# Optimization experiments

Hardware: AMD Instinct MI355X
Metric: run time of the kernel (lower is better)

Reference implementation:

```python
import jax, jax.numpy as jnp
import numpy as np

NUM_HEADS = 16
NUM_EXPERTS = 8
TOP_K = 2
LN_EPS = 1e-5


def _layernorm(x, g, b):
    mu = x.mean(-1, keepdims=True)
    var = ((x - mu) ** 2).mean(-1, keepdims=True)
    return (x - mu) * jax.lax.rsqrt(var + LN_EPS) * g + b


def _rope(x, cos, sin):
    # x: [B,S,H,D]; cos/sin: [S, D//2]; interleaved even/odd pairs
    B, S, H, D = x.shape
    xr = x.reshape(B, S, H, D // 2, 2)
    xe, xo = xr[..., 0], xr[..., 1]
    c = cos[None, :, None, :]
    s = sin[None, :, None, :]
    ye = xe * c - xo * s
    yo = xe * s + xo * c
    return jnp.stack((ye, yo), axis=-1).reshape(B, S, H, D)


def setup_inputs() -> dict:
    key = jax.random.key(0)
    ks = jax.random.split(key, 8)
    B, S, D = 4, 512, 1024
    E, Hd = NUM_EXPERTS, 1792
    sc = 0.02
    return {
        'x': jax.random.normal(ks[0], (B, S, D), jnp.float32),
        'ln1_g': jnp.ones((D,), jnp.float32),
        'ln1_b': jnp.zeros((D,), jnp.float32),
        'ln2_g': jnp.ones((D,), jnp.float32),
        'ln2_b': jnp.zeros((D,), jnp.float32),
        'w_qkv': jax.random.normal(ks[1], (D, 3 * D), jnp.float32) * sc,
        'w_o': jax.random.normal(ks[2], (D, D), jnp.float32) * sc,
        'gate_w': jax.random.normal(ks[3], (D, E), jnp.float32) * sc,
        'w_gate': jax.random.normal(ks[4], (E, D, Hd), jnp.float32) * sc,
        'w_up': jax.random.normal(ks[5], (E, D, Hd), jnp.float32) * sc,
        'w_down': jax.random.normal(ks[6], (E, Hd, D), jnp.float32) * sc,
    }


def reference(x, ln1_g, ln1_b, ln2_g, ln2_b, w_qkv, w_o, gate_w, w_gate, w_up, w_down):
    B, S, D = x.shape
    H = NUM_HEADS
    hd = D // H

    # --- attention with RoPE ---
    xn = _layernorm(x, ln1_g, ln1_b)
    qkv = xn @ w_qkv                      # [B,S,3D]
    q, k, v = jnp.split(qkv, 3, axis=-1)
    q = q.reshape(B, S, H, hd)
    k = k.reshape(B, S, H, hd)
    v = v.reshape(B, S, H, hd)
    inv_freq = 1.0 / (10000.0 ** (jnp.arange(0, hd, 2, dtype=jnp.float32) / hd))
    t = jnp.arange(S, dtype=jnp.float32)
    freqs = jnp.outer(t, inv_freq)        # [S, hd//2]
    cos, sin = jnp.cos(freqs), jnp.sin(freqs)
    q = _rope(q, cos, sin)
    k = _rope(k, cos, sin)
    scale = 1.0 / jnp.sqrt(jnp.asarray(hd, x.dtype))
    scores = jnp.einsum('bshd,bthd->bhst', q, k) * scale
    causal = jnp.tril(jnp.ones((S, S), bool))
    scores = jnp.where(causal[None, None], scores, jnp.finfo(scores.dtype).min)
    attn = jax.nn.softmax(scores, axis=-1)
    attn_out = jnp.einsum('bhst,bthd->bshd', attn, v).reshape(B, S, D)
    x = x + attn_out @ w_o

    # --- MoE ---
    xn2 = _layernorm(x, ln2_g, ln2_b)
    xf = xn2.reshape(-1, D)               # [T, D]
    logits = (xf.astype(jnp.bfloat16) @ gate_w.astype(jnp.bfloat16)).astype(jnp.float32)
    topk_w, topk_i = jax.lax.top_k(logits, TOP_K)
    topk_w = jax.nn.softmax(topk_w, axis=-1)
    probs = jax.nn.softmax(logits, axis=-1)
    expert_dist = probs.mean(0)
    lb_loss = NUM_EXPERTS * (expert_dist ** 2).sum()
    # dense dispatch: combine weights [T,E], zero where not selected (same math as sort/gather/scatter)
    cw = (jax.nn.one_hot(topk_i, NUM_EXPERTS, dtype=xf.dtype) * topk_w[..., None].astype(xf.dtype)).sum(1)
    g = jnp.einsum('td,edh->teh', xf, w_gate)
    u = jnp.einsum('td,edh->teh', xf, w_up)
    h = jax.nn.silu(g) * u
    down = jnp.einsum('teh,ehd->ted', h, w_down)
    moe_out = jnp.einsum('ted,te->td', down, cw).reshape(B, S, D)
    x = x + moe_out
    return (x, lb_loss, expert_dist)
```

## Files before the change

### kernel.cpp

```cpp
#include <hip/hip_runtime.h>
#include <hip/hip_bf16.h>
#include <math.h>

#define B_    4
#define S_    512
#define D_    1024
#define T_    2048
#define H_    16
#define HD_   64
#define E_    8
#define HID_  1792
#define D3_   3072
#define GU_   (2 * HID_)

typedef unsigned short ushort_t;
typedef __bf16 bf16x8 __attribute__((ext_vector_type(8)));
typedef float  floatx4 __attribute__((ext_vector_type(4)));

__device__ inline float bf2f(ushort_t u) {
    return __uint_as_float(((unsigned)u) << 16);
}
__device__ inline ushort_t f2bf(float f) {
    __hip_bfloat16 h = __float2bfloat16(f);
    return __builtin_bit_cast(ushort_t, h);
}

__device__ __forceinline__ void gl2lds16(const ushort_t* g, ushort_t* l) {
    __builtin_amdgcn_global_load_lds(
        (const __attribute__((address_space(1))) void*)g,
        (__attribute__((address_space(3))) void*)l, 16, 0, 0);
}

__global__ __launch_bounds__(256) void transpose_bf16_kernel(
    const float* __restrict__ in, ushort_t* __restrict__ out,
    int R, int C, int mul, int add, long outEstride)
{
    __shared__ float tile[32][33];
    const int bx = blockIdx.x * 32;
    const int by = blockIdx.y * 32;
    const size_t iofs = (size_t)blockIdx.z * R * C;
    const size_t oofs = (size_t)blockIdx.z * outEstride;
    const int tx = threadIdx.x & 31;
    const int ty = threadIdx.x >> 5;
#pragma unroll
    for (int i = 0; i < 4; i++) {
        int r = by + ty + i * 8;
        tile[ty + i * 8][tx] = in[iofs + (size_t)r * C + bx + tx];
    }
    __syncthreads();
#pragma unroll
    for (int i = 0; i < 4; i++) {
        int c = bx + ty + i * 8;
        out[oofs + (size_t)(c * mul + add) * R + by + tx] = f2bf(tile[tx][ty + i * 8]);
    }
}

__global__ __launch_bounds__(256) void ln_kernel(
    const float* __restrict__ x, const float* __restrict__ g,
    const float* __restrict__ b, float* __restrict__ outf,
    ushort_t* __restrict__ outb)
{
    const int t = blockIdx.x;
    const int tid = threadIdx.x;
    const int wave = tid >> 6, lane = tid & 63;
    const float4 v = ((const float4*)(x + (size_t)t * D_))[tid];

    float s = v.x + v.y + v.z + v.w;
#pragma unroll
    for (int off = 32; off; off >>= 1) s += __shfl_xor(s, off);
    __shared__ float red1[4];
    __shared__ float red2[4];
    if (lane == 0) red1[wave] = s;
    __syncthreads();
    const float mu = (red1[0] + red1[1] + red1[2] + red1[3]) * (1.0f / D_);

    const float dx = v.x - mu, dy = v.y - mu, dz = v.z - mu, dw = v.w - mu;
    float vs = dx * dx + dy * dy + dz * dz + dw * dw;
#pragma unroll
    for (int off = 32; off; off >>= 1) vs += __shfl_xor(vs, off);
    if (lane == 0) red2[wave] = vs;
    __syncthreads();
    const float var = (red2[0] + red2[1] + red2[2] + red2[3]) * (1.0f / D_);
    const float rs = 1.0f / sqrtf(var + 1e-5f);

    const float4 gg = ((const float4*)g)[tid];
    const float4 bb = ((const float4*)b)[tid];
    float4 o;
    o.x = dx * rs * gg.x + bb.x;
    o.y = dy * rs * gg.y + bb.y;
    o.z = dz * rs * gg.z + bb.z;
    o.w = dw * rs * gg.w + bb.w;
    if (outf) ((float4*)(outf + (size_t)t * D_))[tid] = o;
    if (outb) {
        ushort4 ob;
        ob.x = f2bf(o.x); ob.y = f2bf(o.y); ob.z = f2bf(o.z); ob.w = f2bf(o.w);
        ((ushort4*)(outb + (size_t)t * D_))[tid] = ob;
    }
}

__global__ __launch_bounds__(256) void sgemm_kernel(
    const float* __restrict__ A, const float* __restrict__ B,
    const float* __restrict__ res, float* __restrict__ C,
    int M, int N, int K)
{
    __shared__ float As[16][132];
    __shared__ float Bs[16][132];
    const int tid = threadIdx.x;
    const int m0 = blockIdx.y * 128, n0 = blockIdx.x * 128;
    const int tx = tid & 15, ty = tid >> 4;

    float acc[8][8] = {};

    const int ar = tid >> 2;
    const int ak = (tid & 3) * 4;
    const int bk = tid >> 4;
    const int bc = (tid & 15) * 4;

    const float* Ap0 = A + (size_t)(m0 + ar) * K + ak;
    const float* Ap1 = A + (size_t)(m0 + 64 + ar) * K + ak;
    const float* Bp  = B + (size_t)bk * N + n0 + bc;

    for (int k0 = 0; k0 < K; k0 += 16) {
        const float4 a0 = *(const float4*)(Ap0 + k0);
        const float4 a1 = *(const float4*)(Ap1 + k0);
        const float4 b0 = *(const float4*)(Bp + (size_t)k0 * N);
        const float4 b1 = *(const float4*)(Bp + (size_t)k0 * N + 64);
        __syncthreads();
        As[ak + 0][ar] = a0.x; As[ak + 1][ar] = a0.y;
        As[ak + 2][ar] = a0.z; As[ak + 3][ar] = a0.w;
        As[ak + 0][64 + ar] = a1.x; As[ak + 1][64 + ar] = a1.y;
        As[ak + 2][64 + ar] = a1.z; As[ak + 3][64 + ar] = a1.w;
        *(float4*)&Bs[bk][bc] = b0;
        *(float4*)&Bs[bk][bc + 64] = b1;
        __syncthreads();
#pragma unroll
        for (int k = 0; k < 16; k++) {
            const float4 av0 = *(const float4*)&As[k][ty * 8];
            const float4 av1 = *(const float4*)&As[k][ty * 8 + 4];
            const float4 bv0 = *(const float4*)&Bs[k][tx * 8];
            const float4 bv1 = *(const float4*)&Bs[k][tx * 8 + 4];
            const float a[8] = {av0.x, av0.y, av0.z, av0.w, av1.x, av1.y, av1.z, av1.w};
            const float b[8] = {bv0.x, bv0.y, bv0.z, bv0.w, bv1.x, bv1.y, bv1.z, bv1.w};
#pragma unroll
            for (int i = 0; i < 8; i++)
#pragma unroll
                for (int j = 0; j < 8; j++)
                    acc[i][j] = fmaf(a[i], b[j], acc[i][j]);
        }
    }

#pragma unroll
    for (int i = 0; i < 8; i++) {
        const int row = m0 + ty * 8 + i;
        const size_t base = (size_t)row * N + n0 + tx * 8;
        float4 o0, o1;
        o0.x = acc[i][0]; o0.y = acc[i][1]; o0.z = acc[i][2]; o0.w = acc[i][3];
        o1.x = acc[i][4]; o1.y = acc[i][5]; o1.z = acc[i][6]; o1.w = acc[i][7];
        if (res) {
            const float4 r0 = *(const float4*)(res + base);
            const float4 r1 = *(const float4*)(res + base + 4);
            o0.x += r0.x; o0.y += r0.y; o0.z += r0.z; o0.w += r0.w;
            o1.x += r1.x; o1.y += r1.y; o1.z += r1.z; o1.w += r1.w;
        }
        *(float4*)(C + base) = o0;
        *(float4*)(C + base + 4) = o1;
    }
}

__global__ __launch_bounds__(256) void gateup_kernel(
    const ushort_t* __restrict__ A, const ushort_t* __restrict__ Bgu,
    ushort_t* __restrict__ Hout)
{
    __shared__ __align__(16) ushort_t As[128 * 32];
    __shared__ __align__(16) ushort_t Bs[128 * 32];
    const int e = blockIdx.z;
    const int col0 = blockIdx.x * 128;
    const int row0 = blockIdx.y * 128;
    const ushort_t* Bt = Bgu + (size_t)e * GU_ * D_;
    ushort_t* Hp = Hout + (size_t)e * T_ * HID_;

    const int tid = threadIdx.x, w = tid >> 6, lane = tid & 63;
    const int lr = lane >> 2, lc = (lane & 3) * 8;
    const int wm = (w >> 1) * 64, wn = (w & 1) * 64;
    const int lm = lane & 15, lq = lane >> 4;

    floatx4 acc[4][4] = {};

    const ushort_t* Ap = A + (size_t)(row0 + w * 16 + lr) * D_ + lc;
    const ushort_t* Bp = Bt + (size_t)(col0 + w * 16 + lr) * D_ + lc;
    ushort_t* lA = As + w * 512;
    ushort_t* lB = Bs + w * 512;

    for (int k0 = 0; k0 < D_; k0 += 32) {
        __syncthreads();
        gl2lds16(Ap + k0, lA);
        gl2lds16(Ap + k0 + (size_t)64 * D_, lA + 2048);
        gl2lds16(Bp + k0, lB);
        gl2lds16(Bp + k0 + (size_t)64 * D_, lB + 2048);
        __syncthreads();
        bf16x8 a[4], b[4];
#pragma unroll
        for (int i = 0; i < 4; i++)
            a[i] = *(const bf16x8*)(As + (wm + i * 16 + lm) * 32 + lq * 8);
#pragma unroll
        for (int j = 0; j < 4; j++)
            b[j] = *(const bf16x8*)(Bs + (wn + j * 16 + lm) * 32 + lq * 8);
#pragma unroll
        for (int i = 0; i < 4; i++)
#pragma unroll
            for (int j = 0; j < 4; j++)
                acc[i][j] = __builtin_amdgcn_mfma_f32_16x16x32_bf16(a[i], b[j], acc[i][j], 0, 0, 0);
    }

#pragma unroll
    for (int i = 0; i < 4; i++)
#pragma unroll
        for (int j = 0; j < 4; j++)
#pragma unroll
            for (int r = 0; r < 4; r++) {
                const float v = acc[i][j][r];
                const float vp = __shfl_xor(v, 1);
                const float g = (lm & 1) ? vp : v;
                const float u = (lm & 1) ? v : vp;
                const float h = g / (1.f + __expf(-g)) * u;
                if (!(lm & 1)) {
                    const int row = row0 + wm + i * 16 + lq * 4 + r;
                    const int col = col0 + wn + j * 16 + lm;
                    Hp[(size_t)row * HID_ + (col >> 1)] = f2bf(h);
                }
            }
}

__global__ __launch_bounds__(256) void down_kernel(
    const ushort_t* __restrict__ Hall, const ushort_t* __restrict__ Wd,
    const float* __restrict__ cw, float* __restrict__ out)
{
    __shared__ __align__(16) ushort_t As[128 * 32];
    __shared__ __align__(16) ushort_t Bs[128 * 32];
    const int e = blockIdx.z;
    const int col0 = blockIdx.x * 128;
    const int row0 = blockIdx.y * 128;
    const ushort_t* A = Hall + (size_t)e * T_ * HID_;
    const ushort_t* Bt = Wd + (size_t)e * D_ * HID_;

    const int tid = threadIdx.x, w = tid >> 6, lane = tid & 63;
    const int lr = lane >> 2, lc = (lane & 3) * 8;
    const int wm = (w >> 1) * 64, wn = (w & 1) * 64;
    const int lm = lane & 15, lq = lane >> 4;

    floatx4 acc[4][4] = {};

    const ushort_t* Ap = A + (size_t)(row0 + w * 16 + lr) * HID_ + lc;
    const ushort_t* Bp = Bt + (size_t)(col0 + w * 16 + lr) * HID_ + lc;
    ushort_t* lA = As + w * 512;
    ushort_t* lB = Bs + w * 512;

    for (int k0 = 0; k0 < HID_; k0 += 32) {
        __syncthreads();
        gl2lds16(Ap + k0, lA);
        gl2lds16(Ap + k0 + (size_t)64 * HID_, lA + 2048);
        gl2lds16(Bp + k0, lB);
        gl2lds16(Bp + k0 + (size_t)64 * HID_, lB + 2048);
        __syncthreads();
        bf16x8 a[4], b[4];
#pragma unroll
        for (int i = 0; i < 4; i++)
            a[i] = *(const bf16x8*)(As + (wm + i * 16 + lm) * 32 + lq * 8);
#pragma unroll
        for (int j = 0; j < 4; j++)
            b[j] = *(const bf16x8*)(Bs + (wn + j * 16 + lm) * 32 + lq * 8);
#pragma unroll
        for (int i = 0; i < 4; i++)
#pragma unroll
            for (int j = 0; j < 4; j++)
                acc[i][j] = __builtin_amdgcn_mfma_f32_16x16x32_bf16(a[i], b[j], acc[i][j], 0, 0, 0);
    }

#pragma unroll
    for (int i = 0; i < 4; i++)
#pragma unroll
        for (int r = 0; r < 4; r++) {
            const int row = row0 + wm + i * 16 + lq * 4 + r;
            const float scale = cw[row * E_ + e];
            if (scale != 0.f) {
#pragma unroll
                for (int j = 0; j < 4; j++) {
                    const int col = col0 + wn + j * 16 + lm;
                    atomicAdd(&out[(size_t)row * D_ + col], scale * acc[i][j][r]);
                }
            }
        }
}

__global__ __launch_bounds__(256) void rope_table_kernel(
    float* __restrict__ ctab, float* __restrict__ stab)
{
    const int i = blockIdx.x * 256 + threadIdx.x;
    if (i >= S_ * 32) return;
    const int s = i >> 5, p = i & 31;
    const double e = (double)(2 * p) / 64.0;
    const float pf = (float)pow(10000.0, e);
    const float invf = 1.0f / pf;
    const float fr = (float)s * invf;
    ctab[i] = (float)cos((double)fr);
    stab[i] = (float)sin((double)fr);
}

__global__ __launch_bounds__(256) void rope_kernel(
    float* __restrict__ qkv, const float* __restrict__ ctab,
    const float* __restrict__ stab)
{
    const int n = blockIdx.x * 256 + threadIdx.x;
    const int pair = n & 31;
    const int h = (n >> 5) & 15;
    const int t = n >> 9;
    const int s = t & (S_ - 1);
    const float c = ctab[s * 32 + pair];
    const float sn = stab[s * 32 + pair];
    const size_t base = (size_t)t * D3_ + h * HD_ + pair * 2;
    float x0 = qkv[base], x1 = qkv[base + 1];
    qkv[base]     = x0 * c - x1 * sn;
    qkv[base + 1] = x0 * sn + x1 * c;
    x0 = qkv[base + D_]; x1 = qkv[base + D_ + 1];
    qkv[base + D_]     = x0 * c - x1 * sn;
    qkv[base + D_ + 1] = x0 * sn + x1 * c;
}

__global__ __launch_bounds__(256) void attn_kernel(
    const float* __restrict__ qkv, float* __restrict__ out)
{
    __shared__ float kbuf[64][65];
    __shared__ float vbuf[64][65];
    __shared__ float qs[32][64];
    __shared__ float ps[4][8][64];

    const int b = blockIdx.z, h = blockIdx.y, qt = blockIdx.x;
    const int tid = threadIdx.x, wave = tid >> 6, lane = tid & 63;
    const int q0 = qt * 32;

    for (int i = tid; i < 32 * 64; i += 256) {
        const int qi = i >> 6, d = i & 63;
        const int t = b * S_ + q0 + qi;
        qs[qi][d] = qkv[(size_t)t * D3_ + h * HD_ + d];
    }

    float m[8], l[8], O[8];
#pragma unroll
    for (int qi = 0; qi < 8; qi++) { m[qi] = -INFINITY; l[qi] = 0.f; O[qi] = 0.f; }

    const int maxS = q0 + 31;
    for (int c0 = 0; c0 <= maxS; c0 += 64) {
        __syncthreads();
        for (int i = tid; i < 64 * 16; i += 256) {
            const int key = i >> 4, d4 = (i & 15) * 4;
            const int t = b * S_ + c0 + key;
            const float4 kv = *(const float4*)(qkv + (size_t)t * D3_ + D_ + h * HD_ + d4);
            const float4 vv = *(const float4*)(qkv + (size_t)t * D3_ + 2 * D_ + h * HD_ + d4);
            kbuf[key][d4 + 0] = kv.x; kbuf[key][d4 + 1] = kv.y;
            kbuf[key][d4 + 2] = kv.z; kbuf[key][d4 + 3] = kv.w;
            vbuf[key][d4 + 0] = vv.x; vbuf[key][d4 + 1] = vv.y;
            vbuf[key][d4 + 2] = vv.z; vbuf[key][d4 + 3] = vv.w;
        }
        __syncthreads();

        const int kglob = c0 + lane;
        float sc[8];
#pragma unroll
        for (int qi = 0; qi < 8; qi++) sc[qi] = 0.f;
#pragma unroll 8
        for (int d = 0; d < 64; d++) {
            const float kv = kbuf[lane][d];
#pragma unroll
            for (int qi = 0; qi < 8; qi++)
                sc[qi] = fmaf(qs[wave * 8 + qi][d], kv, sc[qi]);
        }
#pragma unroll
        for (int qi = 0; qi < 8; qi++) {
            const int s = q0 + wave * 8 + qi;
            float v = (kglob <= s) ? sc[qi] * 0.125f : -INFINITY;
            float cmax = v;
#pragma unroll
            for (int off = 32; off; off >>= 1) cmax = fmaxf(cmax, __shfl_xor(cmax, off));
            const float mnew = fmaxf(m[qi], cmax);
            const float alpha = expf(m[qi] - mnew);
            const float p = (v == -INFINITY) ? 0.f : expf(v - mnew);
            float psum = p;
#pragma unroll
            for (int off = 32; off; off >>= 1) psum += __shfl_xor(psum, off);
            l[qi] = l[qi] * alpha + psum;
            m[qi] = mnew;
            ps[wave][qi][lane] = p;
            sc[qi] = alpha;
        }
#pragma unroll
        for (int qi = 0; qi < 8; qi++) O[qi] *= sc[qi];
#pragma unroll 8
        for (int j = 0; j < 64; j++) {
            const float vv = vbuf[j][lane];
#pragma unroll
            for (int qi = 0; qi < 8; qi++)
                O[qi] = fmaf(ps[wave][qi][j], vv, O[qi]);
        }
    }

#pragma unroll
    for (int qi = 0; qi < 8; qi++) {
        const int t = b * S_ + q0 + wave * 8 + qi;
        out[(size_t)t * D_ + h * HD_ + lane] = O[qi] / l[qi];
    }
}

__global__ __launch_bounds__(256) void copy_f32_kernel(
    const float* __restrict__ in, float* __restrict__ out, int n4)
{
    const int i = blockIdx.x * 256 + threadIdx.x;
    if (i < n4) ((float4*)out)[i] = ((const float4*)in)[i];
}

__global__ __launch_bounds__(64) void gate_kernel(
    const ushort_t* __restrict__ xn2, const float* __restrict__ gate_w,
    float* __restrict__ cw, float* __restrict__ probs)
{
    const int t = blockIdx.x;
    const int lane = threadIdx.x;
    float acc[8] = {0, 0, 0, 0, 0, 0, 0, 0};
    for (int d = lane; d < D_; d += 64) {
        const float xv = bf2f(xn2[(size_t)t * D_ + d]);
        const float4 g0 = ((const float4*)(gate_w + d * 8))[0];
        const float4 g1 = ((const float4*)(gate_w + d * 8))[1];
        acc[0] = fmaf(xv, bf2f(f2bf(g0.x)), acc[0]);
        acc[1] = fmaf(xv, bf2f(f2bf(g0.y)), acc[1]);
        acc[2] = fmaf(xv, bf2f(f2bf(g0.z)), acc[2]);
        acc[3] = fmaf(xv, bf2f(f2bf(g0.w)), acc[3]);
        acc[4] = fmaf(xv, bf2f(f2bf(g1.x)), acc[4]);
        acc[5] = fmaf(xv, bf2f(f2bf(g1.y)), acc[5]);
        acc[6] = fmaf(xv, bf2f(f2bf(g1.z)), acc[6]);
        acc[7] = fmaf(xv, bf2f(f2bf(g1.w)), acc[7]);
    }
#pragma unroll
    for (int e = 0; e < 8; e++) {
#pragma unroll
        for (int off = 32; off; off >>= 1) acc[e] += __shfl_xor(acc[e], off);
        acc[e] = bf2f(f2bf(acc[e]));
    }

    if (lane == 0) {
        int i1 = 0;
        for (int e = 1; e < 8; e++) if (acc[e] > acc[i1]) i1 = e;
        int i2 = (i1 == 0) ? 1 : 0;
        for (int e = 0; e < 8; e++) if (e != i1 && acc[e] > acc[i2]) i2 = e;
        const float e2 = expf(acc[i2] - acc[i1]);
        const float w1 = 1.f / (1.f + e2);
        const float w2 = e2 * w1;
        for (int e = 0; e < 8; e++)
            cw[t * 8 + e] = (e == i1) ? w1 : ((e == i2) ? w2 : 0.f);
        const float mx = acc[i1];
        float se = 0.f, pe[8];
        for (int e = 0; e < 8; e++) { pe[e] = expf(acc[e] - mx); se += pe[e]; }
        const float inv = 1.f / se;
        for (int e = 0; e < 8; e++) probs[t * 8 + e] = pe[e] * inv;
    }
}

__global__ __launch_bounds__(256) void reduce_dist_kernel(
    const float* __restrict__ probs, float* __restrict__ out)
{
    __shared__ float part[256];
    __shared__ float dist8[8];
    const int tid = threadIdx.x;
    const int e = tid & 7, chunk = tid >> 3;
    float s = 0.f;
    for (int t = chunk; t < T_; t += 32) s += probs[t * 8 + e];
    part[tid] = s;
    __syncthreads();
    if (tid < 8) {
        float tot = 0.f;
        for (int c = 0; c < 32; c++) tot += part[c * 8 + tid];
        const float dv = tot * (1.0f / T_);
        dist8[tid] = dv;
        out[(size_t)T_ * D_ + 1 + tid] = dv;
    }
    __syncthreads();
    if (tid == 0) {
        float s2 = 0.f;
        for (int k = 0; k < 8; k++) s2 += dist8[k] * dist8[k];
        out[(size_t)T_ * D_] = (float)E_ * s2;
    }
}

extern "C" void kernel_launch(void* const* d_in, const int* in_sizes, int n_in,
                              void* d_out, int out_size, void* d_ws, size_t ws_size,
                              hipStream_t stream)
{
    const float* x      = (const float*)d_in[0];
    const float* ln1_g  = (const float*)d_in[1];
    const float* ln1_b  = (const float*)d_in[2];
    const float* ln2_g  = (const float*)d_in[3];
    const float* ln2_b  = (const float*)d_in[4];
    const float* w_qkv  = (const float*)d_in[5];
    const float* w_o    = (const float*)d_in[6];
    const float* gate_w = (const float*)d_in[7];
    const float* w_gate = (const float*)d_in[8];
    const float* w_up   = (const float*)d_in[9];
    const float* w_down = (const float*)d_in[10];
    float* out = (float*)d_out;

    char* ws = (char*)d_ws;
    size_t off = 0;
    auto alloc = [&](size_t bytes) { size_t o = off; off += (bytes + 255) & ~(size_t)255; return o; };
    ushort_t* wguT  = (ushort_t*)(ws + alloc((size_t)E_ * GU_ * D_ * 2));
    ushort_t* wdT   = (ushort_t*)(ws + alloc((size_t)E_ * D_ * HID_ * 2));
    float*    xn    = (float*)   (ws + alloc((size_t)T_ * D_ * 4));
    ushort_t* xn2   = (ushort_t*)(ws + alloc((size_t)T_ * D_ * 2));
    float*    cw    = (float*)   (ws + alloc((size_t)T_ * E_ * 4));
    float*    probs = (float*)   (ws + alloc((size_t)T_ * E_ * 4));
    float*    ctab  = (float*)   (ws + alloc((size_t)S_ * 32 * 4));
    float*    stab  = (float*)   (ws + alloc((size_t)S_ * 32 * 4));
    const size_t scratch0 = off;
    float*    qkv   = (float*)   (ws + alloc((size_t)T_ * D3_ * 4));
    float*    attnO = (float*)   (ws + alloc((size_t)T_ * D_ * 4));
    float*    x1    = (float*)   (ws + alloc((size_t)T_ * D_ * 4));
    ushort_t* hbufA = (ushort_t*)(ws + scratch0);
    (void)ws_size; (void)in_sizes; (void)n_in; (void)out_size;

    hipLaunchKernelGGL(transpose_bf16_kernel, dim3(HID_ / 32, D_ / 32, E_), dim3(256), 0, stream,
                       w_gate, wguT, D_, HID_, 2, 0, (long)GU_ * D_);
    hipLaunchKernelGGL(transpose_bf16_kernel, dim3(HID_ / 32, D_ / 32, E_), dim3(256), 0, stream,
                       w_up, wguT, D_, HID_, 2, 1, (long)GU_ * D_);
    hipLaunchKernelGGL(transpose_bf16_kernel, dim3(D_ / 32, HID_ / 32, E_), dim3(256), 0, stream,
                       w_down, wdT, HID_, D_, 1, 0, (long)D_ * HID_);

    hipLaunchKernelGGL(rope_table_kernel, dim3((S_ * 32 + 255) / 256), dim3(256), 0, stream,
                       ctab, stab);

    hipLaunchKernelGGL(ln_kernel, dim3(T_), dim3(256), 0, stream,
                       x, ln1_g, ln1_b, xn, (ushort_t*)nullptr);

    hipLaunchKernelGGL(sgemm_kernel, dim3(D3_ / 128, T_ / 128), dim3(256), 0, stream,
                       xn, w_qkv, (const float*)nullptr, qkv, T_, D3_, D_);

    hipLaunchKernelGGL(rope_kernel, dim3(T_ * H_ * 32 / 256), dim3(256), 0, stream,
                       qkv, ctab, stab);

    hipLaunchKernelGGL(attn_kernel, dim3(S_ / 32, H_, B_), dim3(256), 0, stream, qkv, attnO);

    hipLaunchKernelGGL(sgemm_kernel, dim3(D_ / 128, T_ / 128), dim3(256), 0, stream,
                       attnO, w_o, x, x1, T_, D_, D_);

    hipLaunchKernelGGL(copy_f32_kernel, dim3(T_ * D_ / 4 / 256), dim3(256), 0, stream,
                       x1, out, T_ * D_ / 4);

    hipLaunchKernelGGL(ln_kernel, dim3(T_), dim3(256), 0, stream,
                       x1, ln2_g, ln2_b, (float*)nullptr, xn2);

    hipLaunchKernelGGL(gate_kernel, dim3(T_), dim3(64), 0, stream, xn2, gate_w, cw, probs);
    hipLaunchKernelGGL(reduce_dist_kernel, dim3(1), dim3(256), 0, stream, probs, out);

    hipLaunchKernelGGL(gateup_kernel, dim3(GU_ / 128, T_ / 128, E_), dim3(256), 0, stream,
                       xn2, wguT, hbufA);
    hipLaunchKernelGGL(down_kernel, dim3(D_ / 128, T_ / 128, E_), dim3(256), 0, stream,
                       hbufA, wdT, cw, out);
}
```

Before: 1.026 ms.

## Route MoE tokens with per-expert index lists and retile fp32 SGEMMs

Replaces dense all-experts MoE computation with sparse dispatch. The gate kernel appends each token's top-2 expert assignments to per-expert token and weight lists using atomics. The gate/up and down kernels then gather rows through those lists and exit early for tiles beyond each expert's count, cutting MoE matmul work roughly fourfold. The fp32 SGEMM is also templated on a smaller output tile (64 columns, 128 or 64 rows) to launch more blocks, trading away some register reuse per thread.

Measured after the change: 838.5 us. 1.22x faster.

```diff
diff --git a/kernel.cpp b/kernel.cpp
--- a/kernel.cpp
+++ b/kernel.cpp
@@ -98,87 +98,93 @@
     }
 }
 
+template<int TM>
 __global__ __launch_bounds__(256) void sgemm_kernel(
     const float* __restrict__ A, const float* __restrict__ B,
     const float* __restrict__ res, float* __restrict__ C,
     int M, int N, int K)
 {
-    __shared__ float As[16][132];
-    __shared__ float Bs[16][132];
+    constexpr int RM  = TM / 16;
+    constexpr int TPR = 256 / TM;
+    constexpr int KF  = 16 / TPR;
+    __shared__ float As[16][TM + 4];
+    __shared__ float Bs[16][68];
     const int tid = threadIdx.x;
-    const int m0 = blockIdx.y * 128, n0 = blockIdx.x * 128;
+    const int m0 = blockIdx.y * TM, n0 = blockIdx.x * 64;
     const int tx = tid & 15, ty = tid >> 4;
 
-    float acc[8][8] = {};
-
-    const int ar = tid >> 2;
-    const int ak = (tid & 3) * 4;
+    float acc[RM][4] = {};
+
+    const int arow = tid / TPR;
+    const int akk  = (tid % TPR) * KF;
     const int bk = tid >> 4;
     const int bc = (tid & 15) * 4;
 
-    const float* Ap0 = A + (size_t)(m0 + ar) * K + ak;
-    const float* Ap1 = A + (size_t)(m0 + 64 + ar) * K + ak;
-    const float* Bp  = B + (size_t)bk * N + n0 + bc;
+    const float* Ap = A + (size_t)(m0 + arow) * K + akk;
+    const float* Bp = B + (size_t)bk * N + n0 + bc;
 
     for (int k0 = 0; k0 < K; k0 += 16) {
-        const float4 a0 = *(const float4*)(Ap0 + k0);
-        const float4 a1 = *(const float4*)(Ap1 + k0);
-        const float4 b0 = *(const float4*)(Bp + (size_t)k0 * N);
-        const float4 b1 = *(const float4*)(Bp + (size_t)k0 * N + 64);
-        __syncthreads();
-        As[ak + 0][ar] = a0.x; As[ak + 1][ar] = a0.y;
-        As[ak + 2][ar] = a0.z; As[ak + 3][ar] = a0.w;
-        As[ak + 0][64 + ar] = a1.x; As[ak + 1][64 + ar] = a1.y;
-        As[ak + 2][64 + ar] = a1.z; As[ak + 3][64 + ar] = a1.w;
-        *(float4*)&Bs[bk][bc] = b0;
-        *(float4*)&Bs[bk][bc + 64] = b1;
+        float av[KF];
+#pragma unroll
+        for (int f = 0; f < KF / 4; f++) {
+            const float4 t = *(const float4*)(Ap + k0 + f * 4);
+            av[f * 4 + 0] = t.x; av[f * 4 + 1] = t.y;
+            av[f * 4 + 2] = t.z; av[f * 4 + 3] = t.w;
+        }
+        const float4 bv = *(const float4*)(Bp + (size_t)k0 * N);
+        __syncthreads();
+#pragma unroll
+        for (int i = 0; i < KF; i++) As[akk + i][arow] = av[i];
+        *(float4*)&Bs[bk][bc] = bv;
         __syncthreads();
 #pragma unroll
         for (int k = 0; k < 16; k++) {
-            const float4 av0 = *(const float4*)&As[k][ty * 8];
-            const float4 av1 = *(const float4*)&As[k][ty * 8 + 4];
-            const float4 bv0 = *(const float4*)&Bs[k][tx * 8];
-            const float4 bv1 = *(const float4*)&Bs[k][tx * 8 + 4];
-            const float a[8] = {av0.x, av0.y, av0.z, av0.w, av1.x, av1.y, av1.z, av1.w};
-            const float b[8] = {bv0.x, bv0.y, bv0.z, bv0.w, bv1.x, bv1.y, bv1.z, bv1.w};
-#pragma unroll
-            for (int i = 0; i < 8; i++)
-#pragma unroll
-                for (int j = 0; j < 8; j++)
-                    acc[i][j] = fmaf(a[i], b[j], acc[i][j]);
-        }
-    }
-
-#pragma unroll
-    for (int i = 0; i < 8; i++) {
-        const int row = m0 + ty * 8 + i;
-        const size_t base = (size_t)row * N + n0 + tx * 8;
-        float4 o0, o1;
-        o0.x = acc[i][0]; o0.y = acc[i][1]; o0.z = acc[i][2]; o0.w = acc[i][3];
-        o1.x = acc[i][4]; o1.y = acc[i][5]; o1.z = acc[i][6]; o1.w = acc[i][7];
+            float a[RM];
+#pragma unroll
+            for (int f = 0; f < RM / 4; f++) {
+                const float4 t = *(const float4*)&As[k][ty * RM + f * 4];
+                a[f * 4 + 0] = t.x; a[f * 4 + 1] = t.y;
+                a[f * 4 + 2] = t.z; a[f * 4 + 3] = t.w;
+            }
+            const float4 bb = *(const float4*)&Bs[k][tx * 4];
+            const float bj[4] = {bb.x, bb.y, bb.z, bb.w};
+#pragma unroll
+            for (int i = 0; i < RM; i++)
+#pragma unroll
+                for (int j = 0; j < 4; j++)
+                    acc[i][j] = fmaf(a[i], bj[j], acc[i][j]);
+        }
+    }
+
+#pragma unroll
+    for (int i = 0; i < RM; i++) {
+        const int row = m0 + ty * RM + i;
+        const size_t base = (size_t)row * N + n0 + tx * 4;
+        float4 o;
+        o.x = acc[i][0]; o.y = acc[i][1]; o.z = acc[i][2]; o.w = acc[i][3];
         if (res) {
             const float4 r0 = *(const float4*)(res + base);
-            const float4 r1 = *(const float4*)(res + base + 4);
-            o0.x += r0.x; o0.y += r0.y; o0.z += r0.z; o0.w += r0.w;
-            o1.x += r1.x; o1.y += r1.y; o1.z += r1.z; o1.w += r1.w;
-        }
-        *(float4*)(C + base) = o0;
-        *(float4*)(C + base + 4) = o1;
-    }
-}
-
-__global__ __launch_bounds__(256) void gateup_kernel(
+            o.x += r0.x; o.y += r0.y; o.z += r0.z; o.w += r0.w;
+        }
+        *(float4*)(C + base) = o;
+    }
+}
+
+__global__ __launch_bounds__(256) void gateup_idx_kernel(
     const ushort_t* __restrict__ A, const ushort_t* __restrict__ Bgu,
-    ushort_t* __restrict__ Hout)
-{
+    const int* __restrict__ cnt, const int* __restrict__ tok,
+    ushort_t* __restrict__ Hc)
+{
+    const int e = blockIdx.z;
+    const int cntE = cnt[e];
+    const int row0 = blockIdx.y * 128;
+    if (row0 >= cntE) return;
+    const int col0 = blockIdx.x * 128;
+    const ushort_t* Bt = Bgu + (size_t)e * GU_ * D_;
+    ushort_t* Hp = Hc + (size_t)e * T_ * HID_;
+
     __shared__ __align__(16) ushort_t As[128 * 32];
     __shared__ __align__(16) ushort_t Bs[128 * 32];
-    const int e = blockIdx.z;
-    const int col0 = blockIdx.x * 128;
-    const int row0 = blockIdx.y * 128;
-    const ushort_t* Bt = Bgu + (size_t)e * GU_ * D_;
-    ushort_t* Hp = Hout + (size_t)e * T_ * HID_;
-
     const int tid = threadIdx.x, w = tid >> 6, lane = tid & 63;
     const int lr = lane >> 2, lc = (lane & 3) * 8;
     const int wm = (w >> 1) * 64, wn = (w & 1) * 64;
@@ -186,15 +192,18 @@
 
     floatx4 acc[4][4] = {};
 
-    const ushort_t* Ap = A + (size_t)(row0 + w * 16 + lr) * D_ + lc;
+    int r0c = row0 + w * 16 + lr;  if (r0c > cntE - 1) r0c = cntE - 1;
+    int r1c = row0 + 64 + w * 16 + lr; if (r1c > cntE - 1) r1c = cntE - 1;
+    const ushort_t* Ap0 = A + (size_t)tok[e * T_ + r0c] * D_ + lc;
+    const ushort_t* Ap1 = A + (size_t)tok[e * T_ + r1c] * D_ + lc;
     const ushort_t* Bp = Bt + (size_t)(col0 + w * 16 + lr) * D_ + lc;
     ushort_t* lA = As + w * 512;
     ushort_t* lB = Bs + w * 512;
 
     for (int k0 = 0; k0 < D_; k0 += 32) {
         __syncthreads();
-        gl2lds16(Ap + k0, lA);
-        gl2lds16(Ap + k0 + (size_t)64 * D_, lA + 2048);
+        gl2lds16(Ap0 + k0, lA);
+        gl2lds16(Ap1 + k0, lA + 2048);
         gl2lds16(Bp + k0, lB);
         gl2lds16(Bp + k0 + (size_t)64 * D_, lB + 2048);
         __syncthreads();
@@ -231,18 +240,21 @@
             }
 }
 
-__global__ __launch_bounds__(256) void down_kernel(
-    const ushort_t* __restrict__ Hall, const ushort_t* __restrict__ Wd,
-    const float* __restrict__ cw, float* __restrict__ out)
-{
+__global__ __launch_bounds__(256) void down_idx_kernel(
+    const ushort_t* __restrict__ Hc, const ushort_t* __restrict__ Wd,
+    const int* __restrict__ cnt, const int* __restrict__ tok,
+    const float* __restrict__ wt, float* __restrict__ out)
+{
+    const int e = blockIdx.z;
+    const int cntE = cnt[e];
+    const int row0 = blockIdx.y * 128;
+    if (row0 >= cntE) return;
+    const int col0 = blockIdx.x * 128;
+    const ushort_t* A = Hc + (size_t)e * T_ * HID_;
+    const ushort_t* Bt = Wd + (size_t)e * D_ * HID_;
+
     __shared__ __align__(16) ushort_t As[128 * 32];
     __shared__ __align__(16) ushort_t Bs[128 * 32];
-    const int e = blockIdx.z;
-    const int col0 = blockIdx.x * 128;
-    const int row0 = blockIdx.y * 128;
-    const ushort_t* A = Hall + (size_t)e * T_ * HID_;
-    const ushort_t* Bt = Wd + (size_t)e * D_ * HID_;
-
     const int tid = threadIdx.x, w = tid >> 6, lane = tid & 63;
     const int lr = lane >> 2, lc = (lane & 3) * 8;
     const int wm = (w >> 1) * 64, wn = (w & 1) * 64;
@@ -281,12 +293,13 @@
 #pragma unroll
         for (int r = 0; r < 4; r++) {
             const int row = row0 + wm + i * 16 + lq * 4 + r;
-            const float scale = cw[row * E_ + e];
-            if (scale != 0.f) {
+            if (row < cntE) {
+                const int t = tok[e * T_ + row];
+                const float scale = wt[e * T_ + row];
 #pragma unroll
                 for (int j = 0; j < 4; j++) {
                     const int col = col0 + wn + j * 16 + lm;
-                    atomicAdd(&out[(size_t)row * D_ + col], scale * acc[i][j][r]);
+                    atomicAdd(&out[(size_t)t * D_ + col], scale * acc[i][j][r]);
                 }
             }
         }
@@ -419,7 +432,8 @@
 
 __global__ __launch_bounds__(64) void gate_kernel(
     const ushort_t* __restrict__ xn2, const float* __restrict__ gate_w,
-    float* __restrict__ cw, float* __restrict__ probs)
+    int* __restrict__ cnt, int* __restrict__ tok, float* __restrict__ wt,
+    float* __restrict__ probs)
 {
     const int t = blockIdx.x;
     const int lane = threadIdx.x;
@@ -452,14 +466,21 @@
         const float e2 = expf(acc[i2] - acc[i1]);
         const float w1 = 1.f / (1.f + e2);
         const float w2 = e2 * w1;
-        for (int e = 0; e < 8; e++)
-            cw[t * 8 + e] = (e == i1) ? w1 : ((e == i2) ? w2 : 0.f);
+        const int p1 = atomicAdd(&cnt[i1], 1);
+        tok[i1 * T_ + p1] = t; wt[i1 * T_ + p1] = w1;
+        const int p2 = atomicAdd(&cnt[i2], 1);
+        tok[i2 * T_ + p2] = t; wt[i2 * T_ + p2] = w2;
         const float mx = acc[i1];
         float se = 0.f, pe[8];
         for (int e = 0; e < 8; e++) { pe[e] = expf(acc[e] - mx); se += pe[e]; }
         const float inv = 1.f / se;
         for (int e = 0; e < 8; e++) probs[t * 8 + e] = pe[e] * inv;
     }
+}
+
+__global__ void zero_route_kernel(int* __restrict__ cnt)
+{
+    if (threadIdx.x < 8) cnt[threadIdx.x] = 0;
 }
 
 __global__ __launch_bounds__(256) void reduce_dist_kernel(
@@ -512,15 +533,17 @@
     ushort_t* wdT   = (ushort_t*)(ws + alloc((size_t)E_ * D_ * HID_ * 2));
     float*    xn    = (float*)   (ws + alloc((size_t)T_ * D_ * 4));
     ushort_t* xn2   = (ushort_t*)(ws + alloc((size_t)T_ * D_ * 2));
-    float*    cw    = (float*)   (ws + alloc((size_t)T_ * E_ * 4));
+    int*      cnt   = (int*)     (ws + alloc(64));
+    int*      tok   = (int*)     (ws + alloc((size_t)E_ * T_ * 4));
+    float*    wt    = (float*)   (ws + alloc((size_t)E_ * T_ * 4));
     float*    probs = (float*)   (ws + alloc((size_t)T_ * E_ * 4));
     float*    ctab  = (float*)   (ws + alloc((size_t)S_ * 32 * 4));
     float*    stab  = (float*)   (ws + alloc((size_t)S_ * 32 * 4));
-    const size_t scratch0 = off;
-    float*    qkv   = (float*)   (ws + alloc((size_t)T_ * D3_ * 4));
-    float*    attnO = (float*)   (ws + alloc((size_t)T_ * D_ * 4));
-    float*    x1    = (float*)   (ws + alloc((size_t)T_ * D_ * 4));
-    ushort_t* hbufA = (ushort_t*)(ws + scratch0);
+    const size_t scratch0 = alloc((size_t)E_ * T_ * HID_ * 2);
+    float*    qkv   = (float*)   (ws + scratch0);
+    float*    attnO = (float*)   (ws + scratch0 + (size_t)T_ * D3_ * 4);
+    float*    x1    = (float*)   (ws + scratch0 + (size_t)T_ * D3_ * 4 + (size_t)T_ * D_ * 4);
+    ushort_t* Hc    = (ushort_t*)(ws + scratch0);
     (void)ws_size; (void)in_sizes; (void)n_in; (void)out_size;
 
     hipLaunchKernelGGL(transpose_bf16_kernel, dim3(HID_ / 32, D_ / 32, E_), dim3(256), 0, stream,
@@ -536,7 +559,7 @@
     hipLaunchKernelGGL(ln_kernel, dim3(T_), dim3(256), 0, stream,
                        x, ln1_g, ln1_b, xn, (ushort_t*)nullptr);
 
-    hipLaunchKernelGGL(sgemm_kernel, dim3(D3_ / 128, T_ / 128), dim3(256), 0, stream,
+    hipLaunchKernelGGL((sgemm_kernel<128>), dim3(D3_ / 64, T_ / 128), dim3(256), 0, stream,
                        xn, w_qkv, (const float*)nullptr, qkv, T_, D3_, D_);
 
     hipLaunchKernelGGL(rope_kernel, dim3(T_ * H_ * 32 / 256), dim3(256), 0, stream,
@@ -544,7 +567,7 @@
 
     hipLaunchKernelGGL(attn_kernel, dim3(S_ / 32, H_, B_), dim3(256), 0, stream, qkv, attnO);
 
-    hipLaunchKernelGGL(sgemm_kernel, dim3(D_ / 128, T_ / 128), dim3(256), 0, stream,
+    hipLaunchKernelGGL((sgemm_kernel<64>), dim3(D_ / 64, T_ / 64), dim3(256), 0, stream,
                        attnO, w_o, x, x1, T_, D_, D_);
 
     hipLaunchKernelGGL(copy_f32_kernel, dim3(T_ * D_ / 4 / 256), dim3(256), 0, stream,
@@ -553,11 +576,13 @@
     hipLaunchKernelGGL(ln_kernel, dim3(T_), dim3(256), 0, stream,
                        x1, ln2_g, ln2_b, (float*)nullptr, xn2);
 
-    hipLaunchKernelGGL(gate_kernel, dim3(T_), dim3(64), 0, stream, xn2, gate_w, cw, probs);
+    hipLaunchKernelGGL(zero_route_kernel, dim3(1), dim3(64), 0, stream, cnt);
+    hipLaunchKernelGGL(gate_kernel, dim3(T_), dim3(64), 0, stream,
+                       xn2, gate_w, cnt, tok, wt, probs);
     hipLaunchKernelGGL(reduce_dist_kernel, dim3(1), dim3(256), 0, stream, probs, out);
 
-    hipLaunchKernelGGL(gateup_kernel, dim3(GU_ / 128, T_ / 128, E_), dim3(256), 0, stream,
-                       xn2, wguT, hbufA);
-    hipLaunchKernelGGL(down_kernel, dim3(D_ / 128, T_ / 128, E_), dim3(256), 0, stream,
-                       hbufA, wdT, cw, out);
-}
+    hipLaunchKernelGGL(gateup_idx_kernel, dim3(GU_ / 128, T_ / 128, E_), dim3(256), 0, stream,
+                       xn2, wguT, cnt, tok, Hc);
+    hipLaunchKernelGGL(down_idx_kernel, dim3(D_ / 128, T_ / 128, E_), dim3(256), 0, stream,
+                       Hc, wdT, cnt, tok, wt, out);
+}
```
